# Kernel tuning notes

Measured on AMD Instinct MI355X. Metric: run time of the kernel, lower is better.

Reference implementation:

```python
import jax, jax.numpy as jnp
import numpy as np

E = 65536          # num edges
T = 262144         # num triplets
EMB_EDGE = 512
EMB_RBF = 16
EMB_CBF = 16
EMB_TRI = 64
EMB_BIL = 64
INV_SQRT2 = 1.0 / 2.0 ** 0.5


def setup_inputs() -> dict:
    key = jax.random.key(0)
    ks = jax.random.split(key, 14)
    m_st = jax.random.normal(ks[0], (E, EMB_EDGE), jnp.float32)
    rbf = jax.random.uniform(ks[1], (E, EMB_RBF), jnp.float32)
    cbf = jax.random.uniform(ks[2], (T, EMB_CBF), jnp.float32)
    idx_swap = jax.random.permutation(ks[3], E)
    id3_kt = jax.random.randint(ks[4], (T,), 0, E)
    id3_st = jnp.sort(jax.random.randint(ks[5], (T,), 0, E))
    st_np = np.asarray(id3_st)
    # rank of each triplet within its (sorted) segment
    id3_ragged_idx = jnp.asarray(np.arange(T) - np.searchsorted(st_np, st_np, side='left'))

    def w(k, shape, fan_in):
        return jax.random.normal(k, shape, jnp.float32) / jnp.float32(fan_in) ** 0.5

    W_mkt = w(ks[6], (EMB_EDGE, EMB_EDGE), EMB_EDGE)
    W_rbf = w(ks[7], (EMB_RBF, EMB_EDGE), EMB_RBF)
    W_down = w(ks[8], (EMB_EDGE, EMB_TRI), EMB_EDGE)
    W_bil = w(ks[9], (EMB_CBF, EMB_TRI, EMB_BIL), EMB_CBF * EMB_TRI)
    W_st = w(ks[10], (EMB_BIL, EMB_EDGE), EMB_BIL)
    W_ts = w(ks[11], (EMB_BIL, EMB_EDGE), EMB_BIL)
    s_rbf = jnp.ones((), jnp.float32)   # ScaleFactor (fitted scalar, init 1.0)
    s_cbf = jnp.ones((), jnp.float32)
    return dict(m_st=m_st, rbf=rbf, cbf=cbf, idx_swap=idx_swap, id3_kt=id3_kt,
                id3_st=id3_st, id3_ragged_idx=id3_ragged_idx,
                W_mkt=W_mkt, W_rbf=W_rbf, W_down=W_down, W_bil=W_bil,
                W_st=W_st, W_ts=W_ts, s_rbf=s_rbf, s_cbf=s_cbf)


def reference(m_st, rbf, cbf, idx_swap, id3_kt, id3_st, id3_ragged_idx,
              W_mkt, W_rbf, W_down, W_bil, W_st, W_ts, s_rbf, s_cbf):
    act = jax.nn.silu
    num_edges = m_st.shape[0]
    # edge MLPs (Dense bias=False + activation)
    m_kt = act(m_st @ W_mkt)                       # (E, EMB_EDGE)
    m_kt = (m_kt * (rbf @ W_rbf)) * s_rbf          # rbf modulation + ScaleFactor
    m_kt = act(m_kt @ W_down)                      # (E, EMB_TRI)
    # gather onto triplets
    m_t = m_kt[id3_kt]                             # (T, EMB_TRI)
    # EfficientInteractionBilinear: out[e,o] = sum_{t in seg(e)} cbf[t,i] m_t[t,j] W_bil[i,j,o]
    outer = cbf[:, :, None] * m_t[:, None, :]      # (T, EMB_CBF, EMB_TRI)
    S = jax.ops.segment_sum(outer, id3_st, num_segments=num_edges)  # (E, CBF, TRI)
    x = jnp.einsum('eij,ijo->eo', S, W_bil) * s_cbf  # (E, EMB_BIL), ScaleFactor
    x_st = act(x @ W_st)                           # (E, EMB_EDGE)
    x_ts = act(x @ W_ts)[idx_swap]                 # swapped-edge branch
    return (x_st + x_ts) * INV_SQRT2
```

## Files before the change

kernel.cpp:

```cpp
#include <hip/hip_runtime.h>
#include <hip/hip_bf16.h>

#define E_EDGES 65536
#define T_TRI   262144

typedef __attribute__((ext_vector_type(8))) __bf16 bf16x8;
typedef __attribute__((ext_vector_type(4))) float  f32x4;

__device__ __forceinline__ unsigned short f2bf(float f) {
    union { float f; unsigned u; } v; v.f = f;
    unsigned r = (v.u + 0x7fffu + ((v.u >> 16) & 1u)) >> 16;
    return (unsigned short)r;
}
__device__ __forceinline__ float bf2f(unsigned short u) {
    union { unsigned u; float f; } v; v.u = ((unsigned)u) << 16; return v.f;
}
__device__ __forceinline__ float asf(unsigned u) {
    union { unsigned u; float f; } v; v.u = u; return v.f;
}
__device__ __forceinline__ float silu(float x) { return x / (1.0f + __expf(-x)); }

#define MFMA(a, b, c) __builtin_amdgcn_mfma_f32_16x16x32_bf16((a), (b), (c), 0, 0, 0)

__device__ __forceinline__ void glds16(const void* g, void* l) {
    __builtin_amdgcn_global_load_lds(
        (const __attribute__((address_space(1))) unsigned int*)g,
        (__attribute__((address_space(3))) unsigned int*)l, 16, 0, 0);
}

__global__ __launch_bounds__(256) void k_prep(
    const float* __restrict__ m_st, const float* __restrict__ rbf,
    const int* __restrict__ id3_st,
    const float* __restrict__ W_mkt, const float* __restrict__ W_rbf,
    const float* __restrict__ W_down, const float* __restrict__ W_bil,
    const float* __restrict__ W_st, const float* __restrict__ W_ts,
    unsigned short* __restrict__ Abf, unsigned short* __restrict__ rbfbf,
    unsigned short* __restrict__ Wt, unsigned short* __restrict__ WrbfT,
    unsigned short* __restrict__ Wdt, unsigned short* __restrict__ Wbt,
    unsigned short* __restrict__ Wstt, unsigned short* __restrict__ Wtst,
    int* __restrict__ offs)
{
    int b = blockIdx.x, t = threadIdx.x;
    if (b < 32768) {
        int idx = b * 256 + t;
        float4 v = ((const float4*)m_st)[idx];
        ushort4 p; p.x = f2bf(v.x); p.y = f2bf(v.y); p.z = f2bf(v.z); p.w = f2bf(v.w);
        ((ushort4*)Abf)[idx] = p;
    } else if (b < 40960) {
        int idx = (b - 32768) * 256 + t; int e = idx >> 5, kk = idx & 31;
        rbfbf[idx] = (kk < 16) ? f2bf(rbf[(size_t)e * 16 + kk]) : (unsigned short)0;
    } else if (b < 41984) {
        int idx = (b - 40960) * 256 + t; int n = idx >> 9, k = idx & 511;
        Wt[idx] = f2bf(W_mkt[k * 512 + n]);
    } else if (b < 42240) {
        int idx = (b - 41984) * 256 + t; int n = idx >> 10, k = idx & 1023;
        Wbt[idx] = f2bf(W_bil[k * 64 + n]);
    } else if (b < 42368) {
        int idx = (b - 42240) * 256 + t; int n = idx >> 9, k = idx & 511;
        Wdt[idx] = f2bf(W_down[k * 64 + n]);
    } else if (b < 42496) {
        int idx = (b - 42368) * 256 + t; int n = idx >> 6, k = idx & 63;
        Wstt[idx] = f2bf(W_st[k * 512 + n]);
    } else if (b < 42624) {
        int idx = (b - 42496) * 256 + t; int n = idx >> 6, k = idx & 63;
        Wtst[idx] = f2bf(W_ts[k * 512 + n]);
    } else if (b < 42688) {
        int idx = (b - 42624) * 256 + t; int c = idx >> 5, kk = idx & 31;
        WrbfT[idx] = (kk < 16) ? f2bf(W_rbf[kk * 512 + c]) : (unsigned short)0;
    } else {
        int tt = (b - 42688) * 256 + t;
        if (tt < T_TRI) {
            int s = id3_st[tt];
            if (tt == 0) { for (int e = 0; e <= s; e++) offs[e] = 0; }
            else { int p = id3_st[tt - 1]; for (int e = p + 1; e <= s; e++) offs[e] = tt; }
            if (tt == T_TRI - 1) { for (int e = s + 1; e <= E_EDGES; e++) offs[e] = T_TRI; }
        }
    }
}

__global__ __launch_bounds__(256) void k_gemm1(
    const unsigned short* __restrict__ Abf, const unsigned short* __restrict__ Wt,
    const unsigned short* __restrict__ rbfbf, const unsigned short* __restrict__ WrbfT,
    const float* __restrict__ s_rbf, unsigned short* __restrict__ C1)
{
    __shared__ __align__(16) unsigned short lA[128 * 32];
    __shared__ __align__(16) unsigned short lB[128 * 32];
    const int tid = threadIdx.x;
    const int e0 = (blockIdx.x >> 2) * 128, n0 = (blockIdx.x & 3) * 128;
    const int wave = tid >> 6, lane = tid & 63, quad = lane >> 4, l16 = lane & 15;
    const int wy = wave >> 1, wx = wave & 1;
    const int sr = tid >> 2, sc = (tid & 3) * 8;
    unsigned short* dA0 = &lA[sr * 32 + sc];
    unsigned short* dA1 = &lA[(64 + sr) * 32 + sc];
    unsigned short* dB0 = &lB[sr * 32 + sc];
    unsigned short* dB1 = &lB[(64 + sr) * 32 + sc];

    unsigned pk[4][4][2];
    {
        glds16(rbfbf + (size_t)(e0 + sr) * 32 + sc, dA0);
        glds16(rbfbf + (size_t)(e0 + 64 + sr) * 32 + sc, dA1);
        glds16(WrbfT + (size_t)(n0 + sr) * 32 + sc, dB0);
        glds16(WrbfT + (size_t)(n0 + 64 + sr) * 32 + sc, dB1);
        __syncthreads();
        f32x4 t2[4][4] = {};
        bf16x8 af[4], bq[4];
#pragma unroll
        for (int mt = 0; mt < 4; mt++)
            af[mt] = *(const bf16x8*)&lA[(wy * 64 + mt * 16 + l16) * 32 + quad * 8];
#pragma unroll
        for (int nt = 0; nt < 4; nt++)
            bq[nt] = *(const bf16x8*)&lB[(wx * 64 + nt * 16 + l16) * 32 + quad * 8];
#pragma unroll
        for (int mt = 0; mt < 4; mt++)
#pragma unroll
            for (int nt = 0; nt < 4; nt++) t2[mt][nt] = MFMA(af[mt], bq[nt], t2[mt][nt]);
#pragma unroll
        for (int mt = 0; mt < 4; mt++)
#pragma unroll
            for (int nt = 0; nt < 4; nt++) {
                pk[mt][nt][0] = ((unsigned)f2bf(t2[mt][nt][1]) << 16) | f2bf(t2[mt][nt][0]);
                pk[mt][nt][1] = ((unsigned)f2bf(t2[mt][nt][3]) << 16) | f2bf(t2[mt][nt][2]);
            }
    }

    f32x4 acc[4][4] = {};
    for (int k0 = 0; k0 < 512; k0 += 32) {
        __syncthreads();
        glds16(Abf + (size_t)(e0 + sr) * 512 + k0 + sc, dA0);
        glds16(Abf + (size_t)(e0 + 64 + sr) * 512 + k0 + sc, dA1);
        glds16(Wt + (size_t)(n0 + sr) * 512 + k0 + sc, dB0);
        glds16(Wt + (size_t)(n0 + 64 + sr) * 512 + k0 + sc, dB1);
        __syncthreads();
        bf16x8 af[4], bq[4];
#pragma unroll
        for (int mt = 0; mt < 4; mt++)
            af[mt] = *(const bf16x8*)&lA[(wy * 64 + mt * 16 + l16) * 32 + quad * 8];
#pragma unroll
        for (int nt = 0; nt < 4; nt++)
            bq[nt] = *(const bf16x8*)&lB[(wx * 64 + nt * 16 + l16) * 32 + quad * 8];
#pragma unroll
        for (int mt = 0; mt < 4; mt++)
#pragma unroll
            for (int nt = 0; nt < 4; nt++) acc[mt][nt] = MFMA(af[mt], bq[nt], acc[mt][nt]);
    }

    float srs = *s_rbf;
#pragma unroll
    for (int mt = 0; mt < 4; mt++)
#pragma unroll
        for (int nt = 0; nt < 4; nt++) {
            int row = e0 + wy * 64 + mt * 16 + quad * 4;
            int col = n0 + wx * 64 + nt * 16 + l16;
            float r0 = asf(pk[mt][nt][0] << 16), r1 = asf(pk[mt][nt][0] & 0xffff0000u);
            float r2 = asf(pk[mt][nt][1] << 16), r3 = asf(pk[mt][nt][1] & 0xffff0000u);
            C1[(size_t)(row + 0) * 512 + col] = f2bf(silu(acc[mt][nt][0]) * r0 * srs);
            C1[(size_t)(row + 1) * 512 + col] = f2bf(silu(acc[mt][nt][1]) * r1 * srs);
            C1[(size_t)(row + 2) * 512 + col] = f2bf(silu(acc[mt][nt][2]) * r2 * srs);
            C1[(size_t)(row + 3) * 512 + col] = f2bf(silu(acc[mt][nt][3]) * r3 * srs);
        }
}

__global__ __launch_bounds__(256) void k_gemm2(
    const unsigned short* __restrict__ C1, const unsigned short* __restrict__ Wdt,
    unsigned short* __restrict__ m2bf)
{
    __shared__ __align__(16) unsigned short lA[128 * 32];
    __shared__ __align__(16) unsigned short lB[64 * 32];
    const int tid = threadIdx.x;
    const int e0 = blockIdx.x * 128;
    const int wave = tid >> 6, lane = tid & 63, quad = lane >> 4, l16 = lane & 15;
    const int wy = wave >> 1, wx = wave & 1;
    const int sr = tid >> 2, sc = (tid & 3) * 8;

    f32x4 acc[4][2] = {};
    for (int k0 = 0; k0 < 512; k0 += 32) {
        __syncthreads();
        glds16(C1 + (size_t)(e0 + sr) * 512 + k0 + sc, &lA[sr * 32 + sc]);
        glds16(C1 + (size_t)(e0 + 64 + sr) * 512 + k0 + sc, &lA[(64 + sr) * 32 + sc]);
        glds16(Wdt + (size_t)sr * 512 + k0 + sc, &lB[sr * 32 + sc]);
        __syncthreads();
        bf16x8 af[4], bq[2];
#pragma unroll
        for (int mt = 0; mt < 4; mt++)
            af[mt] = *(const bf16x8*)&lA[(wy * 64 + mt * 16 + l16) * 32 + quad * 8];
#pragma unroll
        for (int nt = 0; nt < 2; nt++)
            bq[nt] = *(const bf16x8*)&lB[(wx * 32 + nt * 16 + l16) * 32 + quad * 8];
#pragma unroll
        for (int mt = 0; mt < 4; mt++)
#pragma unroll
            for (int nt = 0; nt < 2; nt++) acc[mt][nt] = MFMA(af[mt], bq[nt], acc[mt][nt]);
    }
#pragma unroll
    for (int mt = 0; mt < 4; mt++)
#pragma unroll
        for (int nt = 0; nt < 2; nt++) {
            int row = e0 + wy * 64 + mt * 16 + quad * 4;
            int col = wx * 32 + nt * 16 + l16;
#pragma unroll
            for (int j = 0; j < 4; j++)
                m2bf[(size_t)(row + j) * 64 + col] = f2bf(silu(acc[mt][nt][j]));
        }
}

__global__ __launch_bounds__(256) void k_tri(
    const float* __restrict__ cbf, const unsigned short* __restrict__ m2bf,
    const int* __restrict__ id3_kt, const int* __restrict__ offs,
    const unsigned short* __restrict__ Wbt, const float* __restrict__ s_cbf,
    unsigned short* __restrict__ xbf)
{
    __shared__ unsigned short lS[16][1032];
    const int tid = threadIdx.x;
    const int g = tid >> 4, l = tid & 15;
    const int e = blockIdx.x * 16 + g;
    const int lo = offs[e], hi = offs[e + 1];

    float S[16][4];
#pragma unroll
    for (int i = 0; i < 16; i++)
#pragma unroll
        for (int j = 0; j < 4; j++) S[i][j] = 0.f;

    for (int t = lo; t < hi; t++) {
        int kt = id3_kt[t];
        const float4* cp = (const float4*)(cbf + (size_t)t * 16);
        float4 c0 = cp[0], c1 = cp[1], c2 = cp[2], c3 = cp[3];
        ushort4 mv = *(const ushort4*)(m2bf + (size_t)kt * 64 + l * 4);
        float m0 = bf2f(mv.x), m1 = bf2f(mv.y), m2v = bf2f(mv.z), m3 = bf2f(mv.w);
        float cc[16] = {c0.x, c0.y, c0.z, c0.w, c1.x, c1.y, c1.z, c1.w,
                        c2.x, c2.y, c2.z, c2.w, c3.x, c3.y, c3.z, c3.w};
#pragma unroll
        for (int i = 0; i < 16; i++) {
            S[i][0] += cc[i] * m0; S[i][1] += cc[i] * m1;
            S[i][2] += cc[i] * m2v; S[i][3] += cc[i] * m3;
        }
    }
#pragma unroll
    for (int i = 0; i < 16; i++) {
        ushort4 p; p.x = f2bf(S[i][0]); p.y = f2bf(S[i][1]);
        p.z = f2bf(S[i][2]); p.w = f2bf(S[i][3]);
        *(ushort4*)&lS[g][i * 64 + l * 4] = p;
    }
    __syncthreads();

    const int wave = tid >> 6, lane = tid & 63, quad = lane >> 4, l16 = lane & 15;
    f32x4 acc = {};
    const unsigned short* bp = Wbt + (size_t)(wave * 16 + l16) * 1024 + quad * 8;
#pragma unroll
    for (int k0 = 0; k0 < 1024; k0 += 32) {
        bf16x8 a = *(const bf16x8*)&lS[l16][k0 + quad * 8];
        bf16x8 b = *(const bf16x8*)(bp + k0);
        acc = MFMA(a, b, acc);
    }
    float sc = *s_cbf;
#pragma unroll
    for (int j = 0; j < 4; j++) {
        int ee = blockIdx.x * 16 + quad * 4 + j;
        xbf[(size_t)ee * 64 + wave * 16 + l16] = f2bf(acc[j] * sc);
    }
}

__global__ __launch_bounds__(256) void k_out(
    const unsigned short* __restrict__ xbf, const int* __restrict__ idx_swap,
    const unsigned short* __restrict__ Wstt, const unsigned short* __restrict__ Wtst,
    float* __restrict__ out)
{
    __shared__ unsigned short lA1[128][72], lA2[128][72];
    __shared__ unsigned short lB1[64][72], lB2[64][72];
    const int tid = threadIdx.x;
    const int e0 = blockIdx.x * 128, n0 = blockIdx.y * 64;
    {
        int r = tid >> 1, h = tid & 1;
        int rs = idx_swap[e0 + r];
        const uint4* s1 = (const uint4*)(xbf + (size_t)(e0 + r) * 64 + h * 32);
        const uint4* s2 = (const uint4*)(xbf + (size_t)rs * 64 + h * 32);
#pragma unroll
        for (int i = 0; i < 4; i++) {
            *(uint4*)&lA1[r][h * 32 + i * 8] = s1[i];
            *(uint4*)&lA2[r][h * 32 + i * 8] = s2[i];
        }
    }
#pragma unroll
    for (int it = 0; it < 2; it++) {
        int c = tid + it * 256;
        int r = c >> 3, cq = (c & 7) * 8;
        *(uint4*)&lB1[r][cq] = *(const uint4*)(Wstt + (size_t)(n0 + r) * 64 + cq);
        *(uint4*)&lB2[r][cq] = *(const uint4*)(Wtst + (size_t)(n0 + r) * 64 + cq);
    }
    __syncthreads();

    const int wave = tid >> 6, lane = tid & 63, quad = lane >> 4, l16 = lane & 15;
    f32x4 a1[2][4] = {}, a2[2][4] = {};
#pragma unroll
    for (int k0 = 0; k0 < 64; k0 += 32) {
        bf16x8 af1[2], af2[2];
        af1[0] = *(const bf16x8*)&lA1[wave * 32 + l16][k0 + quad * 8];
        af1[1] = *(const bf16x8*)&lA1[wave * 32 + 16 + l16][k0 + quad * 8];
        af2[0] = *(const bf16x8*)&lA2[wave * 32 + l16][k0 + quad * 8];
        af2[1] = *(const bf16x8*)&lA2[wave * 32 + 16 + l16][k0 + quad * 8];
#pragma unroll
        for (int nt = 0; nt < 4; nt++) {
            bf16x8 b1 = *(const bf16x8*)&lB1[nt * 16 + l16][k0 + quad * 8];
            bf16x8 b2 = *(const bf16x8*)&lB2[nt * 16 + l16][k0 + quad * 8];
            a1[0][nt] = MFMA(af1[0], b1, a1[0][nt]);
            a1[1][nt] = MFMA(af1[1], b1, a1[1][nt]);
            a2[0][nt] = MFMA(af2[0], b2, a2[0][nt]);
            a2[1][nt] = MFMA(af2[1], b2, a2[1][nt]);
        }
    }
    const float cs = 0.7071067811865476f;
#pragma unroll
    for (int mt = 0; mt < 2; mt++)
#pragma unroll
        for (int nt = 0; nt < 4; nt++) {
            int rbase = e0 + wave * 32 + mt * 16 + quad * 4;
            int col = n0 + nt * 16 + l16;
#pragma unroll
            for (int j = 0; j < 4; j++)
                out[(size_t)(rbase + j) * 512 + col] =
                    (silu(a1[mt][nt][j]) + silu(a2[mt][nt][j])) * cs;
        }
}

extern "C" void kernel_launch(void* const* d_in, const int* in_sizes, int n_in,
                              void* d_out, int out_size, void* d_ws, size_t ws_size,
                              hipStream_t stream)
{
    const float* m_st   = (const float*)d_in[0];
    const float* rbf    = (const float*)d_in[1];
    const float* cbf    = (const float*)d_in[2];
    const int*   idx_sw = (const int*)d_in[3];
    const int*   id3_kt = (const int*)d_in[4];
    const int*   id3_st = (const int*)d_in[5];
    const float* W_mkt  = (const float*)d_in[7];
    const float* W_rbf  = (const float*)d_in[8];
    const float* W_down = (const float*)d_in[9];
    const float* W_bil  = (const float*)d_in[10];
    const float* W_st   = (const float*)d_in[11];
    const float* W_ts   = (const float*)d_in[12];
    const float* s_rbf  = (const float*)d_in[13];
    const float* s_cbf  = (const float*)d_in[14];
    float* out = (float*)d_out;

    char* ws = (char*)d_ws;
    unsigned short* Abf   = (unsigned short*)(ws);
    unsigned short* m2bf  = (unsigned short*)(ws + 67108864);
    unsigned short* xbf   = (unsigned short*)(ws + 75497472);
    unsigned short* rbfbf = (unsigned short*)(ws + 83886080);
    unsigned short* Wt    = (unsigned short*)(ws + 88080384);
    unsigned short* WrbfT = (unsigned short*)(ws + 88604672);
    unsigned short* Wdt   = (unsigned short*)(ws + 88637440);
    unsigned short* Wbt   = (unsigned short*)(ws + 88702976);
    unsigned short* Wstt  = (unsigned short*)(ws + 88834048);
    unsigned short* Wtst  = (unsigned short*)(ws + 88899584);
    int*            offs  = (int*)(ws + 88965120);
    unsigned short* C1 = (unsigned short*)d_out;

    k_prep<<<43712, 256, 0, stream>>>(m_st, rbf, id3_st,
                                      W_mkt, W_rbf, W_down, W_bil, W_st, W_ts,
                                      Abf, rbfbf, Wt, WrbfT, Wdt, Wbt, Wstt, Wtst, offs);
    k_gemm1<<<2048, 256, 0, stream>>>(Abf, Wt, rbfbf, WrbfT, s_rbf, C1);
    k_gemm2<<<512, 256, 0, stream>>>(C1, Wdt, m2bf);
    k_tri<<<4096, 256, 0, stream>>>(cbf, m2bf, id3_kt, offs, Wbt, s_cbf, xbf);
    k_out<<<dim3(512, 8), 256, 0, stream>>>(xbf, idx_sw, Wstt, Wtst, out);
}
```

Before: 478.1 us.

## Pre-gather triplet features into contiguous buffer and prefetch in triplet loop

Adds a separate gather kernel that copies m2bf rows indexed by id3_kt into a triplet-ordered buffer held in the output scratch region. The triplet loop then streams contiguous data with a one-step software prefetch of cbf and m2t, which removes the dependent index load from the inner loop. The bilinear MFMA loop now uses two independent accumulators to shorten the dependency chain. The cost is an extra kernel launch plus about 32MB of extra write and read traffic for the gathered buffer.

```diff
diff --git a/kernel.cpp b/kernel.cpp
--- a/kernel.cpp
+++ b/kernel.cpp
@@ -203,9 +203,19 @@
         }
 }
 
+__global__ __launch_bounds__(256) void k_gath(
+    const int* __restrict__ id3_kt, const unsigned short* __restrict__ m2bf,
+    unsigned short* __restrict__ m2t)
+{
+    int idx = blockIdx.x * 256 + threadIdx.x;
+    int t = idx >> 3, s = (idx & 7) * 8;
+    int kt = id3_kt[t];
+    *(uint4*)(m2t + (size_t)t * 64 + s) = *(const uint4*)(m2bf + (size_t)kt * 64 + s);
+}
+
 __global__ __launch_bounds__(256) void k_tri(
-    const float* __restrict__ cbf, const unsigned short* __restrict__ m2bf,
-    const int* __restrict__ id3_kt, const int* __restrict__ offs,
+    const float* __restrict__ cbf, const unsigned short* __restrict__ m2t,
+    const int* __restrict__ offs,
     const unsigned short* __restrict__ Wbt, const float* __restrict__ s_cbf,
     unsigned short* __restrict__ xbf)
 {
@@ -221,14 +231,17 @@
 #pragma unroll
         for (int j = 0; j < 4; j++) S[i][j] = 0.f;
 
+    const float4* cp = (const float4*)(cbf + (size_t)lo * 16);
+    const ushort4* mp = (const ushort4*)(m2t + (size_t)lo * 64 + l * 4);
+    float4 a0, a1, a2, a3; ushort4 am;
+    if (lo < hi) { a0 = cp[0]; a1 = cp[1]; a2 = cp[2]; a3 = cp[3]; am = *mp; }
     for (int t = lo; t < hi; t++) {
-        int kt = id3_kt[t];
-        const float4* cp = (const float4*)(cbf + (size_t)t * 16);
-        float4 c0 = cp[0], c1 = cp[1], c2 = cp[2], c3 = cp[3];
-        ushort4 mv = *(const ushort4*)(m2bf + (size_t)kt * 64 + l * 4);
-        float m0 = bf2f(mv.x), m1 = bf2f(mv.y), m2v = bf2f(mv.z), m3 = bf2f(mv.w);
-        float cc[16] = {c0.x, c0.y, c0.z, c0.w, c1.x, c1.y, c1.z, c1.w,
-                        c2.x, c2.y, c2.z, c2.w, c3.x, c3.y, c3.z, c3.w};
+        float4 b0 = a0, b1 = a1, b2 = a2, b3 = a3; ushort4 bm = am;
+        cp += 4; mp += 16;
+        if (t + 1 < hi) { a0 = cp[0]; a1 = cp[1]; a2 = cp[2]; a3 = cp[3]; am = *mp; }
+        float m0 = bf2f(bm.x), m1 = bf2f(bm.y), m2v = bf2f(bm.z), m3 = bf2f(bm.w);
+        float cc[16] = {b0.x, b0.y, b0.z, b0.w, b1.x, b1.y, b1.z, b1.w,
+                        b2.x, b2.y, b2.z, b2.w, b3.x, b3.y, b3.z, b3.w};
 #pragma unroll
         for (int i = 0; i < 16; i++) {
             S[i][0] += cc[i] * m0; S[i][1] += cc[i] * m1;
@@ -244,19 +257,22 @@
     __syncthreads();
 
     const int wave = tid >> 6, lane = tid & 63, quad = lane >> 4, l16 = lane & 15;
-    f32x4 acc = {};
+    f32x4 acc0 = {}, acc1 = {};
     const unsigned short* bp = Wbt + (size_t)(wave * 16 + l16) * 1024 + quad * 8;
 #pragma unroll
-    for (int k0 = 0; k0 < 1024; k0 += 32) {
-        bf16x8 a = *(const bf16x8*)&lS[l16][k0 + quad * 8];
-        bf16x8 b = *(const bf16x8*)(bp + k0);
-        acc = MFMA(a, b, acc);
+    for (int k0 = 0; k0 < 1024; k0 += 64) {
+        bf16x8 a0v = *(const bf16x8*)&lS[l16][k0 + quad * 8];
+        bf16x8 b0v = *(const bf16x8*)(bp + k0);
+        acc0 = MFMA(a0v, b0v, acc0);
+        bf16x8 a1v = *(const bf16x8*)&lS[l16][k0 + 32 + quad * 8];
+        bf16x8 b1v = *(const bf16x8*)(bp + k0 + 32);
+        acc1 = MFMA(a1v, b1v, acc1);
     }
     float sc = *s_cbf;
 #pragma unroll
     for (int j = 0; j < 4; j++) {
         int ee = blockIdx.x * 16 + quad * 4 + j;
-        xbf[(size_t)ee * 64 + wave * 16 + l16] = f2bf(acc[j] * sc);
+        xbf[(size_t)ee * 64 + wave * 16 + l16] = f2bf((acc0[j] + acc1[j]) * sc);
     }
 }
 
@@ -354,13 +370,15 @@
     unsigned short* Wstt  = (unsigned short*)(ws + 88834048);
     unsigned short* Wtst  = (unsigned short*)(ws + 88899584);
     int*            offs  = (int*)(ws + 88965120);
-    unsigned short* C1 = (unsigned short*)d_out;
+    unsigned short* C1  = (unsigned short*)d_out;
+    unsigned short* m2t = (unsigned short*)((char*)d_out + 67108864);
 
     k_prep<<<43712, 256, 0, stream>>>(m_st, rbf, id3_st,
                                       W_mkt, W_rbf, W_down, W_bil, W_st, W_ts,
                                       Abf, rbfbf, Wt, WrbfT, Wdt, Wbt, Wstt, Wtst, offs);
     k_gemm1<<<2048, 256, 0, stream>>>(Abf, Wt, rbfbf, WrbfT, s_rbf, C1);
     k_gemm2<<<512, 256, 0, stream>>>(C1, Wdt, m2bf);
-    k_tri<<<4096, 256, 0, stream>>>(cbf, m2bf, id3_kt, offs, Wbt, s_cbf, xbf);
+    k_gath<<<8192, 256, 0, stream>>>(id3_kt, m2bf, m2t);
+    k_tri<<<4096, 256, 0, stream>>>(cbf, m2t, offs, Wbt, s_cbf, xbf);
     k_out<<<dim3(512, 8), 256, 0, stream>>>(xbf, idx_sw, Wstt, Wtst, out);
 }
```

After: 480.2 us. Within noise of the previous version (+0.4%).
